# Kernel optimization log

Hardware: AMD Instinct MI355X
Metric: run time of the kernel (lower is better)

Reference implementation:

```python
import jax, jax.numpy as jnp
import numpy as np

E = 128      # embedding_dim
H = 64       # hidden_dim
B = 2048     # batch
L = 200      # history length
NEG = -1e30  # stand-in for -inf (avoids NaN for all-pad rows; same math when any key unmasked)


def setup_inputs() -> dict:
    key = jax.random.key(0)
    ks = jax.random.split(key, 10)
    s1 = 1.0 / np.sqrt(4 * E)
    s2 = 1.0 / np.sqrt(H)
    return {
        "query": jax.random.normal(ks[0], (B, E), jnp.float32),
        "keys": jax.random.normal(ks[1], (B, L, E), jnp.float32),
        "mask": jax.random.randint(ks[2], (B, L), 0, 2, jnp.int32),
        "W1": jax.random.uniform(ks[3], (4 * E, H), jnp.float32, -s1, s1),
        "b1": jax.random.uniform(ks[4], (H,), jnp.float32, -s1, s1),
        "W2": jax.random.uniform(ks[5], (H, H), jnp.float32, -s2, s2),
        "b2": jax.random.uniform(ks[6], (H,), jnp.float32, -s2, s2),
        "W3": jax.random.uniform(ks[7], (H, 1), jnp.float32, -s2, s2),
        "b3": jax.random.uniform(ks[8], (1,), jnp.float32, -s2, s2),
        "no_hist": jax.random.normal(ks[9], (E,), jnp.float32) * 0.001,
    }


def reference(query, keys, mask, W1, b1, W2, b2, W3, b3, no_hist):
    # q expanded over L, 4-way concat features: [q, k, q*k, q-k] -> (B, L, 4E)
    q = jnp.broadcast_to(query[:, None, :], keys.shape)
    attn_in = jnp.concatenate([q, keys, q * keys, q - keys], axis=-1)
    # 3-layer MLP scorer -> (B, L)
    h = jax.nn.relu(attn_in @ W1 + b1)
    h = jax.nn.relu(h @ W2 + b2)
    scores = (h @ W3 + b3)[..., 0]
    # masked softmax over L, then zero masked slots and renormalize
    m = mask.astype(scores.dtype)
    scores = jnp.where(m == 0, NEG, scores)
    attn = jax.nn.softmax(scores, axis=1) * m
    denom = jnp.sum(attn, axis=1, keepdims=True)
    attn = attn / (denom + 1e-12)
    # weighted sum of keys -> (B, E)
    user_interest = jnp.einsum("bl,ble->be", attn, keys)
    # rows with no history get the learned no-hist embedding
    all_pad = jnp.sum(m, axis=1) == 0  # (B,)
    user_interest = jnp.where(all_pad[:, None], no_hist[None, :], user_interest)
    return user_interest
```

## Files before the change

kernel.cpp:

```cpp
#include <hip/hip_runtime.h>


#define NB 2048
#define LE 128
#define LH 64
#define LL 200
#define NMT 13

typedef short bf16x8 __attribute__((ext_vector_type(8)));
typedef float f32x4 __attribute__((ext_vector_type(4)));

__device__ __forceinline__ short f2bf(float f) {
  unsigned u = __float_as_uint(f);
  u += 0x7fffu + ((u >> 16) & 1u);
  return (short)(u >> 16);
}

struct __align__(16) SM {
  short keys[208 * 128];
  short h1[4][16 * 72];
  float scores[208];
  float q[128];
  float bias1[64];
  float b2s[64];
  float w3s[64];
  float red[16];
};

__global__ void k0_prep(const float* __restrict__ W1, const float* __restrict__ W2,
                        float* __restrict__ BD, float* __restrict__ Cq,
                        float* __restrict__ AD, short* __restrict__ W2T) {
  int idx = blockIdx.x * 256 + threadIdx.x;
  if (idx < 8192) {
    int h = idx >> 7, e = idx & 127;
    BD[idx] = W1[(128 + e) * LH + h] - W1[(384 + e) * LH + h];
    Cq[idx] = W1[(256 + e) * LH + h];
    int e2 = idx >> 6, h2 = idx & 63;
    AD[idx] = W1[e2 * LH + h2] + W1[(384 + e2) * LH + h2];
    if (idx < 4096) {
      int c = idx >> 6, k = idx & 63;
      W2T[idx] = f2bf(W2[k * LH + c]);
    }
  }
}

__global__ void __launch_bounds__(256, 2)
din_attn(const float* __restrict__ query, const float* __restrict__ keysg,
         const int* __restrict__ mask, const float* __restrict__ b1,
         const float* __restrict__ b2, const float* __restrict__ W3,
         const float* __restrict__ no_hist,
         const float* __restrict__ BD, const float* __restrict__ Cq,
         const float* __restrict__ AD, const short* __restrict__ W2T,
         float* __restrict__ out)
{
  __shared__ SM sm;
  const int b    = blockIdx.x;
  const int t    = threadIdx.x;
  const int lane = t & 63;
  const int wv   = t >> 6;
  const int col  = lane & 15;
  const int quad = lane >> 4;

  int my_mask = 0;
  if (t < LL) my_mask = mask[b * LL + t];
  if (t < LE) sm.q[t] = query[b * LE + t];
  if (t < LH) { sm.b2s[t] = b2[t]; sm.w3s[t] = W3[t]; }
  __syncthreads();

  bf16x8 fB2[4][2];
  #pragma unroll
  for (int n = 0; n < 4; ++n)
    #pragma unroll
    for (int k2 = 0; k2 < 2; ++k2)
      fB2[n][k2] = *(const bf16x8*)&W2T[(n * 16 + col) * 64 + k2 * 32 + quad * 8];

  short* scratch = &sm.keys[0];
  #pragma unroll
  for (int i = 0; i < 4; ++i) {
    int idx = (t + 256 * i) * 8;
    int h = idx >> 7, e0 = idx & 127;
    float4 bd0 = *(const float4*)&BD[idx];
    float4 bd1 = *(const float4*)&BD[idx + 4];
    float4 c0  = *(const float4*)&Cq[idx];
    float4 c1  = *(const float4*)&Cq[idx + 4];
    bf16x8 w;
    w[0] = f2bf(bd0.x + sm.q[e0 + 0] * c0.x);
    w[1] = f2bf(bd0.y + sm.q[e0 + 1] * c0.y);
    w[2] = f2bf(bd0.z + sm.q[e0 + 2] * c0.z);
    w[3] = f2bf(bd0.w + sm.q[e0 + 3] * c0.w);
    w[4] = f2bf(bd1.x + sm.q[e0 + 4] * c1.x);
    w[5] = f2bf(bd1.y + sm.q[e0 + 5] * c1.y);
    w[6] = f2bf(bd1.z + sm.q[e0 + 6] * c1.z);
    w[7] = f2bf(bd1.w + sm.q[e0 + 7] * c1.w);
    *(bf16x8*)&scratch[h * 136 + e0] = w;
  }
  {
    int h = lane;
    float acc = 0.f;
    #pragma unroll 8
    for (int e = wv * 32; e < wv * 32 + 32; ++e)
      acc = fmaf(sm.q[e], AD[e * LH + h], acc);
    float* biasp = (float*)&sm.h1[0][0];
    biasp[wv * 64 + h] = acc;
  }
  __syncthreads();

  bf16x8 fB1[4][4];
  #pragma unroll
  for (int n = 0; n < 4; ++n)
    #pragma unroll
    for (int kt = 0; kt < 4; ++kt)
      fB1[n][kt] = *(const bf16x8*)&scratch[(n * 16 + col) * 136 + kt * 32 + quad * 8];

  if (t < LH) {
    const float* biasp = (const float*)&sm.h1[0][0];
    sm.bias1[t] = b1[t] + biasp[t] + biasp[64 + t] + biasp[128 + t] + biasp[192 + t];
  }
  __syncthreads();

  const float* kb = keysg + (size_t)b * LL * LE;
  short* h1w = &sm.h1[wv][0];

  auto do_tile = [&](int mt) {
    int row = mt * 16 + col;
    int rowg = row < LL ? row : LL - 1;
    const float* rp = kb + rowg * LE;
    bf16x8 a[4];
    #pragma unroll
    for (int kt = 0; kt < 4; ++kt) {
      float4 v0 = *(const float4*)&rp[kt * 32 + quad * 8];
      float4 v1 = *(const float4*)&rp[kt * 32 + quad * 8 + 4];
      bf16x8 av;
      av[0] = f2bf(v0.x); av[1] = f2bf(v0.y); av[2] = f2bf(v0.z); av[3] = f2bf(v0.w);
      av[4] = f2bf(v1.x); av[5] = f2bf(v1.y); av[6] = f2bf(v1.z); av[7] = f2bf(v1.w);
      a[kt] = av;
      *(bf16x8*)&sm.keys[row * 128 + (((kt * 4 + quad) ^ col) * 8)] = av;
    }
    #pragma unroll
    for (int n = 0; n < 4; ++n) {
      f32x4 acc = {0.f, 0.f, 0.f, 0.f};
      #pragma unroll
      for (int kt = 0; kt < 4; ++kt)
        acc = __builtin_amdgcn_mfma_f32_16x16x32_bf16(a[kt], fB1[n][kt], acc, 0, 0, 0);
      float bias = sm.bias1[n * 16 + col];
      #pragma unroll
      for (int i = 0; i < 4; ++i)
        h1w[(quad * 4 + i) * 72 + n * 16 + col] = f2bf(fmaxf(acc[i] + bias, 0.f));
    }
    bf16x8 a2[2];
    #pragma unroll
    for (int k2 = 0; k2 < 2; ++k2)
      a2[k2] = *(const bf16x8*)&h1w[col * 72 + k2 * 32 + quad * 8];
    float p[4] = {0.f, 0.f, 0.f, 0.f};
    #pragma unroll
    for (int n = 0; n < 4; ++n) {
      f32x4 c2 = {0.f, 0.f, 0.f, 0.f};
      c2 = __builtin_amdgcn_mfma_f32_16x16x32_bf16(a2[0], fB2[n][0], c2, 0, 0, 0);
      c2 = __builtin_amdgcn_mfma_f32_16x16x32_bf16(a2[1], fB2[n][1], c2, 0, 0, 0);
      float bb = sm.b2s[n * 16 + col];
      float w3 = sm.w3s[n * 16 + col];
      #pragma unroll
      for (int i = 0; i < 4; ++i)
        p[i] = fmaf(fmaxf(c2[i] + bb, 0.f), w3, p[i]);
    }
    #pragma unroll
    for (int i = 0; i < 4; ++i) {
      #pragma unroll
      for (int off = 1; off < 16; off <<= 1)
        p[i] += __shfl_xor(p[i], off);
      if (col == 0) sm.scores[mt * 16 + quad * 4 + i] = p[i];
    }
  };

  do_tile(wv);
  do_tile(wv + 4);
  do_tile(wv + 8);
  if (wv == 0) do_tile(12);
  __syncthreads();

  float sc = (t < LL) ? sm.scores[t] : -3.0e38f;
  float vmax = (my_mask != 0) ? sc : -3.0e38f;
  #pragma unroll
  for (int off = 1; off < 64; off <<= 1) vmax = fmaxf(vmax, __shfl_xor(vmax, off));
  if (lane == 0) sm.red[wv] = vmax;
  __syncthreads();
  float M = fmaxf(fmaxf(sm.red[0], sm.red[1]), fmaxf(sm.red[2], sm.red[3]));
  float ex = (t < LL && my_mask != 0) ? __expf(sc - M) : 0.f;
  float vsum = ex;
  #pragma unroll
  for (int off = 1; off < 64; off <<= 1) vsum += __shfl_xor(vsum, off);
  if (lane == 0) sm.red[4 + wv] = vsum;
  __syncthreads();
  float Z = sm.red[4] + sm.red[5] + sm.red[6] + sm.red[7];
  bool allpad = !(Z > 0.f);
  float rz = allpad ? 0.f : (1.f / Z);
  if (t < 208) sm.scores[t] = (t < LL) ? ex * rz : 0.f;
  __syncthreads();

  {
    const int part = t >> 5;
    const int ei = (t & 31) * 4;
    float a0 = 0.f, a1 = 0.f, a2s = 0.f, a3 = 0.f;
    int l0 = part * 25;
    #pragma unroll 5
    for (int li = 0; li < 25; ++li) {
      int l = l0 + li;
      float aw = sm.scores[l];
      int blk = (ei >> 3) ^ (l & 15);
      const short* kp = &sm.keys[l * 128 + blk * 8 + (ei & 7)];
      int2 kv = *(const int2*)kp;
      unsigned kx = (unsigned)kv.x, ky = (unsigned)kv.y;
      a0  = fmaf(aw, __uint_as_float(kx << 16), a0);
      a1  = fmaf(aw, __uint_as_float(kx & 0xffff0000u), a1);
      a2s = fmaf(aw, __uint_as_float(ky << 16), a2s);
      a3  = fmaf(aw, __uint_as_float(ky & 0xffff0000u), a3);
    }
    float* redf = (float*)&sm.h1[0][0];
    *(float4*)&redf[part * 128 + ei] = make_float4(a0, a1, a2s, a3);
    __syncthreads();
    if (t < LE) {
      float s = 0.f;
      #pragma unroll
      for (int pp = 0; pp < 8; ++pp) s += redf[pp * 128 + t];
      if (allpad) s = no_hist[t];
      out[b * LE + t] = s;
    }
  }
}

extern "C" void kernel_launch(void* const* d_in, const int* in_sizes, int n_in,
                              void* d_out, int out_size, void* d_ws, size_t ws_size,
                              hipStream_t stream) {
  (void)in_sizes; (void)n_in; (void)ws_size; (void)out_size;
  const float* query   = (const float*)d_in[0];
  const float* keysg   = (const float*)d_in[1];
  const int*   mask    = (const int*)d_in[2];
  const float* W1      = (const float*)d_in[3];
  const float* b1      = (const float*)d_in[4];
  const float* W2      = (const float*)d_in[5];
  const float* b2      = (const float*)d_in[6];
  const float* W3      = (const float*)d_in[7];
  const float* no_hist = (const float*)d_in[9];

  float* BD  = (float*)d_ws;
  float* Cq  = BD + 8192;
  float* AD  = Cq + 8192;
  short* W2T = (short*)(AD + 8192);

  k0_prep<<<32, 256, 0, stream>>>(W1, W2, BD, Cq, AD, W2T);
  din_attn<<<NB, 256, 0, stream>>>(query, keysg, mask, b1, b2, W3, no_hist,
                                   BD, Cq, AD, W2T, (float*)d_out);
}
```

Before: 327.9 us.

## Double-buffer key tiles via async global-to-LDS loads and keep keys in registers

Key rows are now fetched with global_load_lds into per-wave double-buffered fp32 staging areas in shared memory, with the next tile's fetch issued while the current tile's MLP runs. Converted bf16 key fragments stay in registers, so the weighted sum over keys is done from registers with shuffle reductions instead of re-reading a full bf16 key copy in LDS. This aims to hide global load latency and cut LDS traffic, at the cost of much higher register pressure (16 bf16x8 fragments per lane) and more shuffle work in the final reduction.

```diff
diff --git a/kernel.cpp b/kernel.cpp
--- a/kernel.cpp
+++ b/kernel.cpp
@@ -5,7 +5,6 @@
 #define LE 128
 #define LH 64
 #define LL 200
-#define NMT 13
 
 typedef short bf16x8 __attribute__((ext_vector_type(8)));
 typedef float f32x4 __attribute__((ext_vector_type(4)));
@@ -16,8 +15,17 @@
   return (short)(u >> 16);
 }
 
+__device__ __forceinline__ void gll16(const void* g, void* l) {
+  __builtin_amdgcn_global_load_lds(
+      (const __attribute__((address_space(1))) void*)g,
+      (__attribute__((address_space(3))) void*)l, 16, 0, 0);
+}
+
 struct __align__(16) SM {
-  short keys[208 * 128];
+  union {
+    float stag[4][2][16 * 128];
+    short scratch[64 * 136];
+  } u;
   short h1[4][16 * 72];
   float scores[208];
   float q[128];
@@ -60,6 +68,8 @@
   const int wv   = t >> 6;
   const int col  = lane & 15;
   const int quad = lane >> 4;
+  const int l31  = lane & 31;
+  const int lh   = lane >> 5;
 
   int my_mask = 0;
   if (t < LL) my_mask = mask[b * LL + t];
@@ -74,7 +84,7 @@
     for (int k2 = 0; k2 < 2; ++k2)
       fB2[n][k2] = *(const bf16x8*)&W2T[(n * 16 + col) * 64 + k2 * 32 + quad * 8];
 
-  short* scratch = &sm.keys[0];
+  short* scratch = &sm.u.scratch[0];
   #pragma unroll
   for (int i = 0; i < 4; ++i) {
     int idx = (t + 256 * i) * 8;
@@ -120,22 +130,36 @@
 
   const float* kb = keysg + (size_t)b * LL * LE;
   short* h1w = &sm.h1[wv][0];
-
-  auto do_tile = [&](int mt) {
-    int row = mt * 16 + col;
-    int rowg = row < LL ? row : LL - 1;
-    const float* rp = kb + rowg * LE;
-    bf16x8 a[4];
+  const int mts[4] = {wv, wv + 4, wv + 8, 12};
+  const int nt = (wv == 0) ? 4 : 3;
+  float* stg0 = &sm.u.stag[wv][0][0];
+  float* stg1 = &sm.u.stag[wv][1][0];
+
+  auto issue_tile = [&](float* dst, int mt) {
+    #pragma unroll
+    for (int i = 0; i < 8; ++i) {
+      int rl  = 2 * i + lh;
+      int row = mt * 16 + rl;
+      row = row < LL ? row : LL - 1;
+      const float* src = kb + row * LE + ((l31 ^ (rl & 7)) << 2);
+      gll16(src, dst + i * 256);
+    }
+  };
+
+  auto load_frags = [&](const float* sb, bf16x8 (&a)[4]) {
     #pragma unroll
     for (int kt = 0; kt < 4; ++kt) {
-      float4 v0 = *(const float4*)&rp[kt * 32 + quad * 8];
-      float4 v1 = *(const float4*)&rp[kt * 32 + quad * 8 + 4];
+      const int b0 = kt * 8 + quad * 2;
+      float4 v0 = *(const float4*)&sb[col * 128 + ((b0 ^ (col & 7)) << 2)];
+      float4 v1 = *(const float4*)&sb[col * 128 + (((b0 + 1) ^ (col & 7)) << 2)];
       bf16x8 av;
       av[0] = f2bf(v0.x); av[1] = f2bf(v0.y); av[2] = f2bf(v0.z); av[3] = f2bf(v0.w);
       av[4] = f2bf(v1.x); av[5] = f2bf(v1.y); av[6] = f2bf(v1.z); av[7] = f2bf(v1.w);
       a[kt] = av;
-      *(bf16x8*)&sm.keys[row * 128 + (((kt * 4 + quad) ^ col) * 8)] = av;
-    }
+    }
+  };
+
+  auto compute_tile = [&](const bf16x8 (&a)[4], int mt) {
     #pragma unroll
     for (int n = 0; n < 4; ++n) {
       f32x4 acc = {0.f, 0.f, 0.f, 0.f};
@@ -144,8 +168,8 @@
         acc = __builtin_amdgcn_mfma_f32_16x16x32_bf16(a[kt], fB1[n][kt], acc, 0, 0, 0);
       float bias = sm.bias1[n * 16 + col];
       #pragma unroll
-      for (int i = 0; i < 4; ++i)
-        h1w[(quad * 4 + i) * 72 + n * 16 + col] = f2bf(fmaxf(acc[i] + bias, 0.f));
+      for (int j = 0; j < 4; ++j)
+        h1w[(quad * 4 + j) * 72 + n * 16 + col] = f2bf(fmaxf(acc[j] + bias, 0.f));
     }
     bf16x8 a2[2];
     #pragma unroll
@@ -160,22 +184,36 @@
       float bb = sm.b2s[n * 16 + col];
       float w3 = sm.w3s[n * 16 + col];
       #pragma unroll
-      for (int i = 0; i < 4; ++i)
-        p[i] = fmaf(fmaxf(c2[i] + bb, 0.f), w3, p[i]);
-    }
-    #pragma unroll
-    for (int i = 0; i < 4; ++i) {
+      for (int j = 0; j < 4; ++j)
+        p[j] = fmaf(fmaxf(c2[j] + bb, 0.f), w3, p[j]);
+    }
+    #pragma unroll
+    for (int j = 0; j < 4; ++j) {
       #pragma unroll
       for (int off = 1; off < 16; off <<= 1)
-        p[i] += __shfl_xor(p[i], off);
-      if (col == 0) sm.scores[mt * 16 + quad * 4 + i] = p[i];
+        p[j] += __shfl_xor(p[j], off);
+      if (col == 0) sm.scores[mt * 16 + quad * 4 + j] = p[j];
     }
   };
 
-  do_tile(wv);
-  do_tile(wv + 4);
-  do_tile(wv + 8);
-  if (wv == 0) do_tile(12);
+  issue_tile(stg0, mts[0]);
+  issue_tile(stg1, mts[1]);
+
+  bf16x8 ka[4][4];
+  #pragma unroll
+  for (int i = 0; i < 4; ++i) {
+    if (i < nt) {
+      if (i < nt - 1) asm volatile("s_waitcnt vmcnt(8)" ::: "memory");
+      else            asm volatile("s_waitcnt vmcnt(0)" ::: "memory");
+      __builtin_amdgcn_sched_barrier(0);
+      load_frags((i & 1) ? stg1 : stg0, ka[i]);
+      asm volatile("s_waitcnt lgkmcnt(0)" ::: "memory");
+      __builtin_amdgcn_sched_barrier(0);
+      if (i + 2 < nt) issue_tile((i & 1) ? stg1 : stg0, mts[i + 2]);
+      __builtin_amdgcn_sched_barrier(0);
+      compute_tile(ka[i], mts[i]);
+    }
+  }
   __syncthreads();
 
   float sc = (t < LL) ? sm.scores[t] : -3.0e38f;
@@ -198,30 +236,42 @@
   __syncthreads();
 
   {
-    const int part = t >> 5;
-    const int ei = (t & 31) * 4;
-    float a0 = 0.f, a1 = 0.f, a2s = 0.f, a3 = 0.f;
-    int l0 = part * 25;
-    #pragma unroll 5
-    for (int li = 0; li < 25; ++li) {
-      int l = l0 + li;
-      float aw = sm.scores[l];
-      int blk = (ei >> 3) ^ (l & 15);
-      const short* kp = &sm.keys[l * 128 + blk * 8 + (ei & 7)];
-      int2 kv = *(const int2*)kp;
-      unsigned kx = (unsigned)kv.x, ky = (unsigned)kv.y;
-      a0  = fmaf(aw, __uint_as_float(kx << 16), a0);
-      a1  = fmaf(aw, __uint_as_float(kx & 0xffff0000u), a1);
-      a2s = fmaf(aw, __uint_as_float(ky << 16), a2s);
-      a3  = fmaf(aw, __uint_as_float(ky & 0xffff0000u), a3);
-    }
+    float aw[4] = {0.f, 0.f, 0.f, 0.f};
+    #pragma unroll
+    for (int i = 0; i < 4; ++i)
+      if (i < nt) aw[i] = sm.scores[mts[i] * 16 + col];
+
     float* redf = (float*)&sm.h1[0][0];
-    *(float4*)&redf[part * 128 + ei] = make_float4(a0, a1, a2s, a3);
+    #pragma unroll
+    for (int kt = 0; kt < 4; ++kt) {
+      float s[8] = {0.f, 0.f, 0.f, 0.f, 0.f, 0.f, 0.f, 0.f};
+      #pragma unroll
+      for (int i = 0; i < 4; ++i) {
+        if (i < nt) {
+          const int* kv = (const int*)&ka[i][kt];
+          #pragma unroll
+          for (int w = 0; w < 4; ++w) {
+            unsigned u = (unsigned)kv[w];
+            s[2 * w]     = fmaf(aw[i], __uint_as_float(u << 16), s[2 * w]);
+            s[2 * w + 1] = fmaf(aw[i], __uint_as_float(u & 0xffff0000u), s[2 * w + 1]);
+          }
+        }
+      }
+      #pragma unroll
+      for (int j = 0; j < 8; ++j) {
+        #pragma unroll
+        for (int off = 1; off < 16; off <<= 1)
+          s[j] += __shfl_xor(s[j], off);
+      }
+      if (col == 0) {
+        #pragma unroll
+        for (int j = 0; j < 8; ++j)
+          redf[wv * 128 + kt * 32 + quad * 8 + j] = s[j];
+      }
+    }
     __syncthreads();
     if (t < LE) {
-      float s = 0.f;
-      #pragma unroll
-      for (int pp = 0; pp < 8; ++pp) s += redf[pp * 128 + t];
+      float s = redf[t] + redf[128 + t] + redf[256 + t] + redf[384 + t];
       if (allpad) s = no_hist[t];
       out[b * LE + t] = s;
     }
```

New measurement: 328.0 us. About the same (+0.0%).
